# Kernel optimization log

Measured on AMD Instinct MI355X. Metric: run time of the kernel, lower is better.

## Reference

```python
import jax, jax.numpy as jnp
import numpy as np

B, S, HID = 4, 2048, 1024
NH = 16
HD = HID // NH  # 64

def setup_inputs() -> dict:
    key = jax.random.key(0)
    ks = jax.random.split(key, 4)
    scale = 1.0 / np.sqrt(HID)
    return {
        "hidden_states": jax.random.normal(ks[0], (B, S, HID), jnp.float32),
        "attention_mask": jnp.zeros((B, 1, 1, S), jnp.float32),
        "Wq": jax.random.normal(ks[1], (HID, HID), jnp.float32) * scale,
        "bq": jnp.zeros((HID,), jnp.float32),
        "Wk": jax.random.normal(ks[2], (HID, HID), jnp.float32) * scale,
        "bk": jnp.zeros((HID,), jnp.float32),
        "Wv": jax.random.normal(ks[3], (HID, HID), jnp.float32) * scale,
        "bv": jnp.zeros((HID,), jnp.float32),
    }

def _split_heads(x):
    # [B,S,HID] -> [B,NH,S,HD]
    return x.reshape(B, S, NH, HD).transpose(0, 2, 1, 3)

def reference(hidden_states, attention_mask, Wq, bq, Wk, bk, Wv, bv):
    q = _split_heads(hidden_states @ Wq + bq)
    k = _split_heads(hidden_states @ Wk + bk)
    v = _split_heads(hidden_states @ Wv + bv)
    # scores: [B,NH,S,S]
    scores = jnp.einsum("bhqd,bhkd->bhqk", q, k) / jnp.sqrt(jnp.float32(HD))
    scores = scores + attention_mask
    probs = jax.nn.softmax(scores, axis=-1)
    # dropout prob = 0.0 -> identity
    ctx = jnp.einsum("bhqk,bhkd->bhqd", probs, v)
    # [B,NH,S,HD] -> [B,S,HID]
    return ctx.transpose(0, 2, 1, 3).reshape(B, S, HID)
```

## Files before the change

### kernel.cpp

```cpp
#include <hip/hip_runtime.h>
#include <stdint.h>


typedef float  f32x4  __attribute__((ext_vector_type(4)));
typedef short  short8 __attribute__((ext_vector_type(8)));
typedef unsigned short u16;
typedef u16    u16x4  __attribute__((ext_vector_type(4)));
typedef u16    u16x8  __attribute__((ext_vector_type(8)));

#define MFMA_BF16_16x16x32 __builtin_amdgcn_mfma_f32_16x16x32_bf16

#define GLD16(gp, sp)                                                          \
  __builtin_amdgcn_global_load_lds(                                            \
      (const __attribute__((address_space(1))) void*)(gp),                     \
      (__attribute__((address_space(3))) void*)(sp), 16, 0, 0)

__device__ __forceinline__ u16 f2bf(float f) {
  unsigned u = __float_as_uint(f);
  return (u16)((u + 0x7FFFu + ((u >> 16) & 1u)) >> 16);
}

__global__ __launch_bounds__(256) void conv_x_k(const float* __restrict__ x,
                                                u16* __restrict__ xb) {
  const int i = (blockIdx.x * 256 + threadIdx.x) * 4;
  const f32x4 v = *(const f32x4*)(x + i);
  u16x4 o;
#pragma unroll
  for (int j = 0; j < 4; ++j) o[j] = f2bf(v[j]);
  *(u16x4*)(xb + i) = o;
}

__global__ __launch_bounds__(256) void wtrans_k(const float* __restrict__ Wq,
                                                const float* __restrict__ Wk,
                                                const float* __restrict__ Wv,
                                                u16* __restrict__ Wt) {
  const int bx = blockIdx.x;
  const int z = bx >> 9;
  const float* W = (z == 0) ? Wq : ((z == 1) ? Wk : Wv);
  const int r = ((bx & 511) << 8) | threadIdx.x;
  const int kc = r >> 10;
  const int n = r & 1023;
  u16x8 o;
#pragma unroll
  for (int j = 0; j < 8; ++j) o[j] = f2bf(W[(kc * 8 + j) * 1024 + n]);
  *(u16x8*)(Wt + (size_t)z * 1048576 + n * 1024 + kc * 8) = o;
}

__global__ __launch_bounds__(256) void qkv_gemm(
    const u16* __restrict__ Xb, const u16* __restrict__ Wt,
    const float* __restrict__ bq, const float* __restrict__ bk,
    const float* __restrict__ bv, u16* __restrict__ qkv) {
  __shared__ u16 Alds[4096];
  __shared__ u16 Blds[4096];
  const int tid = threadIdx.x;
  const int l = tid & 63, w = tid >> 6;
  const int c = l & 15, g = l >> 4;
  const int nz = blockIdx.x;
  const int z = nz >> 3;
  const int bn = (nz & 7) << 7;
  const int bm = blockIdx.y << 7;
  const u16* wz = Wt + (size_t)z * 1048576;
  const float* bias = (z == 0) ? bq : ((z == 1) ? bk : bv);

  const int srow = l >> 2;
  const int scel = ((l & 3) ^ ((l >> 3) & 3)) << 3;
  const u16* ag = Xb + (size_t)(bm + 32 * w + srow) * 1024 + scel;
  const u16* bg = wz + (size_t)(bn + 32 * w + srow) * 1024 + scel;
  u16* ad = Alds + w * 1024;
  u16* bd = Blds + w * 1024;

  const int m0w = (w >> 1) * 64, n0w = (w & 1) * 64;
  const int swz = ((c >> 1) & 3) << 4;

  f32x4 acc[4][4] = {};

  for (int kk = 0; kk < 1024; kk += 32) {
    __syncthreads();
    GLD16(ag + kk, ad);
    GLD16(ag + kk + 16 * 1024, ad + 512);
    GLD16(bg + kk, bd);
    GLD16(bg + kk + 16 * 1024, bd + 512);
    asm volatile("s_waitcnt vmcnt(0)" ::: "memory");
    __syncthreads();

    short8 af[4], bf[4];
#pragma unroll
    for (int i = 0; i < 4; ++i) {
      const int off = (m0w + 16 * i + c) * 64 + ((g << 4) ^ swz);
      af[i] = *(const short8*)((const char*)Alds + off);
    }
#pragma unroll
    for (int j = 0; j < 4; ++j) {
      const int off = (n0w + 16 * j + c) * 64 + ((g << 4) ^ swz);
      bf[j] = *(const short8*)((const char*)Blds + off);
    }
#pragma unroll
    for (int i = 0; i < 4; ++i)
#pragma unroll
      for (int j = 0; j < 4; ++j)
        acc[i][j] = MFMA_BF16_16x16x32(af[i], bf[j], acc[i][j], 0, 0, 0);
  }

  u16* outz = qkv + (size_t)z * 8388608;
#pragma unroll
  for (int j = 0; j < 4; ++j) {
    const int n = bn + n0w + 16 * j + c;
    const float bvv = bias[n];
    const int hoff = (n >> 6) * 131072;
    const int d = n & 63;
#pragma unroll
    for (int i = 0; i < 4; ++i) {
      const int mb = bm + m0w + 16 * i + 4 * g;
#pragma unroll
      for (int r = 0; r < 4; ++r) {
        const int m = mb + r;
        const float val = acc[i][j][r] + bvv;
        int idx = (m >> 11) * 2097152 + hoff;
        if (z < 2) idx += (m & 2047) * 64 + d;
        else       idx += d * 2048 + (m & 2047);
        outz[idx] = f2bf(val);
      }
    }
  }
}

__global__ __launch_bounds__(256) void attn_fwd(const u16* __restrict__ Qg,
                                                const u16* __restrict__ Kg,
                                                const u16* __restrict__ VTg,
                                                const float* __restrict__ mask,
                                                float* __restrict__ out) {
  __shared__ u16 Klds[2048];
  __shared__ u16 Vlds[2048];
  const int tid = threadIdx.x;
  const int l = tid & 63, w = tid >> 6;
  const int c = l & 15, g = l >> 4;
  const int hb = blockIdx.y, b = hb >> 4, h = hb & 15;
  const int q0 = blockIdx.x * 128 + w * 32;

  const u16* Qh = Qg + (size_t)hb * 131072;
  const u16* Kh = Kg + (size_t)hb * 131072;
  const u16* Vh = VTg + (size_t)hb * 131072;
  const float* mrow = mask + b * 2048;

  short8 qf[2][2];
#pragma unroll
  for (int sub = 0; sub < 2; ++sub)
#pragma unroll
    for (int ks = 0; ks < 2; ++ks)
      qf[sub][ks] =
          *(const short8*)(Qh + (q0 + sub * 16 + c) * 64 + ks * 32 + g * 8);

  f32x4 ctx[2][4] = {};
  float m_run[2] = {-1e30f, -1e30f};
  float l_run[2] = {0.f, 0.f};

  const int krow = 8 * w + (l >> 3);
  const int kcel =
      ((((l & 7) << 4) ^ (((l >> 3) & 3) << 4) ^ ((w & 1) << 6)) >> 1);
  const u16* kg = Kh + krow * 64 + kcel;
  u16* ksd = Klds + w * 512;
  const int vrow = 16 * w + (l >> 2);
  const int vcel = ((((l & 3) ^ ((l >> 3) & 3)) << 4) >> 1);
  const u16* vg = Vh + vrow * 2048 + vcel;
  u16* vsd = Vlds + w * 512;

  const int r0 = 8 * (c >> 2) + (c & 3);
  const int swk = ((c & 3) << 4) | (((c >> 2) & 1) << 6);
  const int swv = ((c >> 1) & 3) << 4;

  for (int it = 0; it < 64; ++it) {
    const int key0 = it << 5;
    __syncthreads();
    GLD16(kg + key0 * 64, ksd);
    GLD16(vg + key0, vsd);
    asm volatile("s_waitcnt vmcnt(0)" ::: "memory");
    __syncthreads();

    short8 af[2][2];
#pragma unroll
    for (int f = 0; f < 2; ++f) {
      const int row = r0 + 4 * f;
#pragma unroll
      for (int ks = 0; ks < 2; ++ks) {
        const int off = row * 128 + (((g << 4) + (ks << 6)) ^ swk);
        af[f][ks] = *(const short8*)((const char*)Klds + off);
      }
    }
    short8 vf[4];
#pragma unroll
    for (int t = 0; t < 4; ++t) {
      const int off = (16 * t + c) * 64 + ((g << 4) ^ swv);
      vf[t] = *(const short8*)((const char*)Vlds + off);
    }
    const f32x4 mv0 = *(const f32x4*)(mrow + key0 + 8 * g);
    const f32x4 mv1 = *(const f32x4*)(mrow + key0 + 8 * g + 4);

#pragma unroll
    for (int sub = 0; sub < 2; ++sub) {
      f32x4 s0 = {0.f, 0.f, 0.f, 0.f}, s1 = {0.f, 0.f, 0.f, 0.f};
      s0 = MFMA_BF16_16x16x32(af[0][0], qf[sub][0], s0, 0, 0, 0);
      s0 = MFMA_BF16_16x16x32(af[0][1], qf[sub][1], s0, 0, 0, 0);
      s1 = MFMA_BF16_16x16x32(af[1][0], qf[sub][0], s1, 0, 0, 0);
      s1 = MFMA_BF16_16x16x32(af[1][1], qf[sub][1], s1, 0, 0, 0);
      float sc[8];
#pragma unroll
      for (int r = 0; r < 4; ++r) {
        sc[r] = s0[r] * 0.125f + mv0[r];
        sc[r + 4] = s1[r] * 0.125f + mv1[r];
      }
      float mx = sc[0];
#pragma unroll
      for (int jj = 1; jj < 8; ++jj) mx = fmaxf(mx, sc[jj]);
      mx = fmaxf(mx, __shfl_xor(mx, 16));
      mx = fmaxf(mx, __shfl_xor(mx, 32));
      const float mnew = fmaxf(m_run[sub], mx);
      const float corr = __expf(m_run[sub] - mnew);
      m_run[sub] = mnew;
      float ls = 0.f;
      short8 p8;
#pragma unroll
      for (int jj = 0; jj < 8; ++jj) {
        const float p = __expf(sc[jj] - mnew);
        ls += p;
        p8[jj] = (short)f2bf(p);
      }
      ls += __shfl_xor(ls, 16);
      ls += __shfl_xor(ls, 32);
      l_run[sub] = l_run[sub] * corr + ls;
#pragma unroll
      for (int t = 0; t < 4; ++t) {
        ctx[sub][t] *= corr;
        ctx[sub][t] = MFMA_BF16_16x16x32(vf[t], p8, ctx[sub][t], 0, 0, 0);
      }
    }
  }

#pragma unroll
  for (int sub = 0; sub < 2; ++sub) {
    const float inv = 1.0f / l_run[sub];
    float* op = out + ((size_t)(b * 2048 + q0 + sub * 16 + c)) * 1024 +
                h * 64 + 4 * g;
#pragma unroll
    for (int t = 0; t < 4; ++t) {
      f32x4 o = ctx[sub][t] * inv;
      *(f32x4*)(op + t * 16) = o;
    }
  }
}

extern "C" void kernel_launch(void* const* d_in, const int* in_sizes, int n_in,
                              void* d_out, int out_size, void* d_ws,
                              size_t ws_size, hipStream_t stream) {
  (void)in_sizes; (void)n_in; (void)out_size; (void)ws_size;
  const float* hidden = (const float*)d_in[0];
  const float* mask = (const float*)d_in[1];
  const float* Wq = (const float*)d_in[2];
  const float* bq = (const float*)d_in[3];
  const float* Wk = (const float*)d_in[4];
  const float* bk = (const float*)d_in[5];
  const float* Wv = (const float*)d_in[6];
  const float* bv = (const float*)d_in[7];
  float* out = (float*)d_out;
  char* ws = (char*)d_ws;
  u16* xbf = (u16*)(ws);
  u16* wt = (u16*)(ws + 16777216);
  u16* qkv = (u16*)(ws + 23068672);

  hipLaunchKernelGGL(conv_x_k, dim3(8192), dim3(256), 0, stream, hidden, xbf);
  hipLaunchKernelGGL(wtrans_k, dim3(1536), dim3(256), 0, stream, Wq, Wk, Wv, wt);
  hipLaunchKernelGGL(qkv_gemm, dim3(24, 64), dim3(256), 0, stream, xbf, wt, bq,
                     bk, bv, qkv);
  hipLaunchKernelGGL(attn_fwd, dim3(16, 64), dim3(256), 0, stream, qkv,
                     qkv + 8388608, qkv + 16777216, mask, out);
}
```

Measured before the change: 339.3 us.

## Double-buffer attention K/V, use exp2 with lazy rescale, widen GEMM K-tile

The QKV GEMM now stages a 64-wide K slice per iteration, which halves the number of barriers, and uses an 8-way XOR swizzle. The V output is written with vectorized 4-element stores. The attention kernel double-buffers K/V tiles in LDS so the next tile's global loads overlap compute. The softmax is moved to base-2 by pre-scaling the mask in a small kernel and folding log2(e) into the score scale. The running max is only rescaled when it grows by more than 8, and packed bf16 conversion is used. Risks: the lazy rescale threshold bounds p at 2^8, and mask2 reuses the weight workspace region after the GEMM has finished reading it.

```diff
diff --git a/kernel.cpp b/kernel.cpp
--- a/kernel.cpp
+++ b/kernel.cpp
@@ -7,6 +7,7 @@
 typedef unsigned short u16;
 typedef u16    u16x4  __attribute__((ext_vector_type(4)));
 typedef u16    u16x8  __attribute__((ext_vector_type(8)));
+typedef unsigned int u32x4 __attribute__((ext_vector_type(4)));
 
 #define MFMA_BF16_16x16x32 __builtin_amdgcn_mfma_f32_16x16x32_bf16
 
@@ -18,6 +19,20 @@
 __device__ __forceinline__ u16 f2bf(float f) {
   unsigned u = __float_as_uint(f);
   return (u16)((u + 0x7FFFu + ((u >> 16) & 1u)) >> 16);
+}
+
+__device__ __forceinline__ unsigned cvt_pk_bf16(float lo, float hi) {
+  unsigned r;
+  asm("v_cvt_pk_bf16_f32 %0, %1, %2" : "=v"(r) : "v"(lo), "v"(hi));
+  return r;
+}
+
+__device__ __forceinline__ float exp2fast(float x) {
+#if __has_builtin(__builtin_amdgcn_exp2f)
+  return __builtin_amdgcn_exp2f(x);
+#else
+  return exp2f(x);
+#endif
 }
 
 __global__ __launch_bounds__(256) void conv_x_k(const float* __restrict__ x,
@@ -46,12 +61,19 @@
   *(u16x8*)(Wt + (size_t)z * 1048576 + n * 1024 + kc * 8) = o;
 }
 
+__global__ __launch_bounds__(256) void mask_k(const float* __restrict__ m,
+                                              float* __restrict__ m2) {
+  const int i = (blockIdx.x * 256 + threadIdx.x) * 4;
+  f32x4 v = *(const f32x4*)(m + i);
+  *(f32x4*)(m2 + i) = v * 1.4426950408889634f;
+}
+
 __global__ __launch_bounds__(256) void qkv_gemm(
     const u16* __restrict__ Xb, const u16* __restrict__ Wt,
     const float* __restrict__ bq, const float* __restrict__ bk,
     const float* __restrict__ bv, u16* __restrict__ qkv) {
-  __shared__ u16 Alds[4096];
-  __shared__ u16 Blds[4096];
+  __shared__ u16 Alds[8192];
+  __shared__ u16 Blds[8192];
   const int tid = threadIdx.x;
   const int l = tid & 63, w = tid >> 6;
   const int c = l & 15, g = l >> 4;
@@ -62,63 +84,86 @@
   const u16* wz = Wt + (size_t)z * 1048576;
   const float* bias = (z == 0) ? bq : ((z == 1) ? bk : bv);
 
-  const int srow = l >> 2;
-  const int scel = ((l & 3) ^ ((l >> 3) & 3)) << 3;
-  const u16* ag = Xb + (size_t)(bm + 32 * w + srow) * 1024 + scel;
-  const u16* bg = wz + (size_t)(bn + 32 * w + srow) * 1024 + scel;
-  u16* ad = Alds + w * 1024;
-  u16* bd = Blds + w * 1024;
+  const int srow = l >> 3;
+  const int sq = ((l & 7) ^ srow) << 3;
+  const u16* ag = Xb + (size_t)(bm + 32 * w + srow) * 1024 + sq;
+  const u16* bg = wz + (size_t)(bn + 32 * w + srow) * 1024 + sq;
+  u16* ad = Alds + w * 2048;
+  u16* bd = Blds + w * 2048;
 
   const int m0w = (w >> 1) * 64, n0w = (w & 1) * 64;
-  const int swz = ((c >> 1) & 3) << 4;
+  const int swq = (c & 7) << 4;
 
   f32x4 acc[4][4] = {};
 
-  for (int kk = 0; kk < 1024; kk += 32) {
+  for (int kk = 0; kk < 1024; kk += 64) {
     __syncthreads();
-    GLD16(ag + kk, ad);
-    GLD16(ag + kk + 16 * 1024, ad + 512);
-    GLD16(bg + kk, bd);
-    GLD16(bg + kk + 16 * 1024, bd + 512);
+#pragma unroll
+    for (int n = 0; n < 4; ++n) {
+      GLD16(ag + kk + n * 8192, ad + n * 512);
+      GLD16(bg + kk + n * 8192, bd + n * 512);
+    }
     asm volatile("s_waitcnt vmcnt(0)" ::: "memory");
     __syncthreads();
 
-    short8 af[4], bf[4];
-#pragma unroll
-    for (int i = 0; i < 4; ++i) {
-      const int off = (m0w + 16 * i + c) * 64 + ((g << 4) ^ swz);
-      af[i] = *(const short8*)((const char*)Alds + off);
-    }
+    short8 af[4][2], bf[4][2];
+#pragma unroll
+    for (int i = 0; i < 4; ++i)
+#pragma unroll
+      for (int ks = 0; ks < 2; ++ks)
+        af[i][ks] = *(const short8*)((const char*)Alds +
+                                     (m0w + 16 * i + c) * 128 +
+                                     (((ks << 6) | (g << 4)) ^ swq));
+#pragma unroll
+    for (int j = 0; j < 4; ++j)
+#pragma unroll
+      for (int ks = 0; ks < 2; ++ks)
+        bf[j][ks] = *(const short8*)((const char*)Blds +
+                                     (n0w + 16 * j + c) * 128 +
+                                     (((ks << 6) | (g << 4)) ^ swq));
+#pragma unroll
+    for (int ks = 0; ks < 2; ++ks)
+#pragma unroll
+      for (int i = 0; i < 4; ++i)
+#pragma unroll
+        for (int j = 0; j < 4; ++j)
+          acc[i][j] = MFMA_BF16_16x16x32(af[i][ks], bf[j][ks], acc[i][j], 0, 0, 0);
+  }
+
+  u16* outz = qkv + (size_t)z * 8388608;
+  if (z == 2) {
 #pragma unroll
     for (int j = 0; j < 4; ++j) {
-      const int off = (n0w + 16 * j + c) * 64 + ((g << 4) ^ swz);
-      bf[j] = *(const short8*)((const char*)Blds + off);
-    }
-#pragma unroll
-    for (int i = 0; i < 4; ++i)
-#pragma unroll
-      for (int j = 0; j < 4; ++j)
-        acc[i][j] = MFMA_BF16_16x16x32(af[i], bf[j], acc[i][j], 0, 0, 0);
-  }
-
-  u16* outz = qkv + (size_t)z * 8388608;
-#pragma unroll
-  for (int j = 0; j < 4; ++j) {
-    const int n = bn + n0w + 16 * j + c;
-    const float bvv = bias[n];
-    const int hoff = (n >> 6) * 131072;
-    const int d = n & 63;
-#pragma unroll
-    for (int i = 0; i < 4; ++i) {
-      const int mb = bm + m0w + 16 * i + 4 * g;
-#pragma unroll
-      for (int r = 0; r < 4; ++r) {
-        const int m = mb + r;
-        const float val = acc[i][j][r] + bvv;
-        int idx = (m >> 11) * 2097152 + hoff;
-        if (z < 2) idx += (m & 2047) * 64 + d;
-        else       idx += d * 2048 + (m & 2047);
-        outz[idx] = f2bf(val);
+      const int n = bn + n0w + 16 * j + c;
+      const float bvv = bias[n];
+      const int hoff = (n >> 6) * 131072;
+      const int d = n & 63;
+#pragma unroll
+      for (int i = 0; i < 4; ++i) {
+        const int mb = bm + m0w + 16 * i + 4 * g;
+        u16x4 o4;
+#pragma unroll
+        for (int r = 0; r < 4; ++r) o4[r] = f2bf(acc[i][j][r] + bvv);
+        *(u16x4*)(outz + (size_t)((mb >> 11) * 2097152 + hoff + d * 2048 +
+                                  (mb & 2047))) = o4;
+      }
+    }
+  } else {
+#pragma unroll
+    for (int j = 0; j < 4; ++j) {
+      const int n = bn + n0w + 16 * j + c;
+      const float bvv = bias[n];
+      const int hoff = (n >> 6) * 131072;
+      const int d = n & 63;
+#pragma unroll
+      for (int i = 0; i < 4; ++i) {
+        const int mb = bm + m0w + 16 * i + 4 * g;
+#pragma unroll
+        for (int r = 0; r < 4; ++r) {
+          const int m = mb + r;
+          outz[(m >> 11) * 2097152 + hoff + (m & 2047) * 64 + d] =
+              f2bf(acc[i][j][r] + bvv);
+        }
       }
     }
   }
@@ -127,20 +172,21 @@
 __global__ __launch_bounds__(256) void attn_fwd(const u16* __restrict__ Qg,
                                                 const u16* __restrict__ Kg,
                                                 const u16* __restrict__ VTg,
-                                                const float* __restrict__ mask,
+                                                const float* __restrict__ mask2,
                                                 float* __restrict__ out) {
-  __shared__ u16 Klds[2048];
-  __shared__ u16 Vlds[2048];
+  __shared__ u16 Klds[2][2048];
+  __shared__ u16 Vlds[2][2048];
   const int tid = threadIdx.x;
   const int l = tid & 63, w = tid >> 6;
   const int c = l & 15, g = l >> 4;
   const int hb = blockIdx.y, b = hb >> 4, h = hb & 15;
   const int q0 = blockIdx.x * 128 + w * 32;
+  const float SCL = 0.1803368801111601f;
 
   const u16* Qh = Qg + (size_t)hb * 131072;
   const u16* Kh = Kg + (size_t)hb * 131072;
   const u16* Vh = VTg + (size_t)hb * 131072;
-  const float* mrow = mask + b * 2048;
+  const float* mrow = mask2 + b * 2048;
 
   short8 qf[2][2];
 #pragma unroll
@@ -158,23 +204,27 @@
   const int kcel =
       ((((l & 7) << 4) ^ (((l >> 3) & 3) << 4) ^ ((w & 1) << 6)) >> 1);
   const u16* kg = Kh + krow * 64 + kcel;
-  u16* ksd = Klds + w * 512;
   const int vrow = 16 * w + (l >> 2);
   const int vcel = ((((l & 3) ^ ((l >> 3) & 3)) << 4) >> 1);
   const u16* vg = Vh + vrow * 2048 + vcel;
-  u16* vsd = Vlds + w * 512;
 
   const int r0 = 8 * (c >> 2) + (c & 3);
   const int swk = ((c & 3) << 4) | (((c >> 2) & 1) << 6);
   const int swv = ((c >> 1) & 3) << 4;
 
+  GLD16(kg, Klds[0] + (w << 9));
+  GLD16(vg, Vlds[0] + (w << 9));
+  asm volatile("s_waitcnt vmcnt(0)" ::: "memory");
+  __syncthreads();
+
   for (int it = 0; it < 64; ++it) {
-    const int key0 = it << 5;
-    __syncthreads();
-    GLD16(kg + key0 * 64, ksd);
-    GLD16(vg + key0, vsd);
-    asm volatile("s_waitcnt vmcnt(0)" ::: "memory");
-    __syncthreads();
+    const int cur = it & 1;
+    const u16* Kb = Klds[cur];
+    const u16* Vb = Vlds[cur];
+    if (it < 63) {
+      GLD16(kg + (it + 1) * 2048, Klds[cur ^ 1] + (w << 9));
+      GLD16(vg + (it + 1) * 32, Vlds[cur ^ 1] + (w << 9));
+    }
 
     short8 af[2][2];
 #pragma unroll
@@ -183,17 +233,17 @@
 #pragma unroll
       for (int ks = 0; ks < 2; ++ks) {
         const int off = row * 128 + (((g << 4) + (ks << 6)) ^ swk);
-        af[f][ks] = *(const short8*)((const char*)Klds + off);
+        af[f][ks] = *(const short8*)((const char*)Kb + off);
       }
     }
     short8 vf[4];
 #pragma unroll
     for (int t = 0; t < 4; ++t) {
       const int off = (16 * t + c) * 64 + ((g << 4) ^ swv);
-      vf[t] = *(const short8*)((const char*)Vlds + off);
-    }
-    const f32x4 mv0 = *(const f32x4*)(mrow + key0 + 8 * g);
-    const f32x4 mv1 = *(const f32x4*)(mrow + key0 + 8 * g + 4);
+      vf[t] = *(const short8*)((const char*)Vb + off);
+    }
+    const f32x4 mv0 = *(const f32x4*)(mrow + (it << 5) + 8 * g);
+    const f32x4 mv1 = *(const f32x4*)(mrow + (it << 5) + 8 * g + 4);
 
 #pragma unroll
     for (int sub = 0; sub < 2; ++sub) {
@@ -205,34 +255,45 @@
       float sc[8];
 #pragma unroll
       for (int r = 0; r < 4; ++r) {
-        sc[r] = s0[r] * 0.125f + mv0[r];
-        sc[r + 4] = s1[r] * 0.125f + mv1[r];
-      }
-      float mx = sc[0];
-#pragma unroll
-      for (int jj = 1; jj < 8; ++jj) mx = fmaxf(mx, sc[jj]);
+        sc[r] = s0[r] * SCL + mv0[r];
+        sc[r + 4] = s1[r] * SCL + mv1[r];
+      }
+      float mx = fmaxf(fmaxf(fmaxf(sc[0], sc[1]), fmaxf(sc[2], sc[3])),
+                       fmaxf(fmaxf(sc[4], sc[5]), fmaxf(sc[6], sc[7])));
       mx = fmaxf(mx, __shfl_xor(mx, 16));
       mx = fmaxf(mx, __shfl_xor(mx, 32));
-      const float mnew = fmaxf(m_run[sub], mx);
-      const float corr = __expf(m_run[sub] - mnew);
-      m_run[sub] = mnew;
+      if (!__all(mx <= m_run[sub] + 8.f)) {
+        const float mnew = fmaxf(m_run[sub], mx);
+        const float corr = exp2fast(m_run[sub] - mnew);
+        m_run[sub] = mnew;
+        l_run[sub] *= corr;
+#pragma unroll
+        for (int t = 0; t < 4; ++t) ctx[sub][t] *= corr;
+      }
+      const float mcur = m_run[sub];
+      float p[8];
       float ls = 0.f;
-      short8 p8;
 #pragma unroll
       for (int jj = 0; jj < 8; ++jj) {
-        const float p = __expf(sc[jj] - mnew);
-        ls += p;
-        p8[jj] = (short)f2bf(p);
+        p[jj] = exp2fast(sc[jj] - mcur);
+        ls += p[jj];
       }
       ls += __shfl_xor(ls, 16);
       ls += __shfl_xor(ls, 32);
-      l_run[sub] = l_run[sub] * corr + ls;
-#pragma unroll
-      for (int t = 0; t < 4; ++t) {
-        ctx[sub][t] *= corr;
+      l_run[sub] += ls;
+      u32x4 pu;
+      pu[0] = cvt_pk_bf16(p[0], p[1]);
+      pu[1] = cvt_pk_bf16(p[2], p[3]);
+      pu[2] = cvt_pk_bf16(p[4], p[5]);
+      pu[3] = cvt_pk_bf16(p[6], p[7]);
+      const short8 p8 = __builtin_bit_cast(short8, pu);
+#pragma unroll
+      for (int t = 0; t < 4; ++t)
         ctx[sub][t] = MFMA_BF16_16x16x32(vf[t], p8, ctx[sub][t], 0, 0, 0);
-      }
-    }
+    }
+
+    asm volatile("s_waitcnt vmcnt(0)" ::: "memory");
+    __syncthreads();
   }
 
 #pragma unroll
@@ -264,12 +325,14 @@
   char* ws = (char*)d_ws;
   u16* xbf = (u16*)(ws);
   u16* wt = (u16*)(ws + 16777216);
+  float* mask2 = (float*)(ws + 16777216);
   u16* qkv = (u16*)(ws + 23068672);
 
   hipLaunchKernelGGL(conv_x_k, dim3(8192), dim3(256), 0, stream, hidden, xbf);
   hipLaunchKernelGGL(wtrans_k, dim3(1536), dim3(256), 0, stream, Wq, Wk, Wv, wt);
   hipLaunchKernelGGL(qkv_gemm, dim3(24, 64), dim3(256), 0, stream, xbf, wt, bq,
                      bk, bv, qkv);
+  hipLaunchKernelGGL(mask_k, dim3(8), dim3(256), 0, stream, mask, mask2);
   hipLaunchKernelGGL(attn_fwd, dim3(16, 64), dim3(256), 0, stream, qkv,
-                     qkv + 8388608, qkv + 16777216, mask, out);
-}
+                     qkv + 8388608, qkv + 16777216, mask2, out);
+}
```

Measured after the change: 309.3 us. 8.8% less time.
